# Performance work log

Measured on AMD Instinct MI355X. Metric: run time of the kernel, lower is better.

## Reference

```python
import jax, jax.numpy as jnp
import numpy as np

N = 50000      # nodes
E = 800000     # edges
IN = 64        # in_feats
HID = 4        # hidden_size
OUT = 64       # out_feats
COORS = 3
EPS = 1e-07
NEG_SLOPE = 0.01  # F.leaky_relu default


def setup_inputs() -> dict:
    key = jax.random.key(0)
    ks = jax.random.split(key, 10)
    feat = jax.random.normal(ks[0], (N, IN), dtype=jnp.float32)
    pos = jax.random.normal(ks[1], (N, COORS), dtype=jnp.float32)
    src = jax.random.randint(ks[2], (E,), 0, N, dtype=jnp.int32)
    dst = jax.random.randint(ks[3], (E,), 0, N, dtype=jnp.int32)
    W_self = jax.random.normal(ks[4], (OUT, IN), dtype=jnp.float32) * 0.1
    W_sp = jax.random.normal(ks[5], (HID * IN, COORS), dtype=jnp.float32) * 0.3
    b_sp = jax.random.normal(ks[6], (HID * IN,), dtype=jnp.float32) * 0.05
    W_neigh = jax.random.normal(ks[7], (OUT, HID * IN), dtype=jnp.float32) * 0.05
    b_neigh = jax.random.normal(ks[8], (OUT,), dtype=jnp.float32) * 0.05
    bias = jnp.zeros((OUT,), dtype=jnp.float32)
    return {"feat": feat, "pos": pos, "src": src, "dst": dst,
            "W_self": W_self, "W_sp": W_sp, "b_sp": b_sp,
            "W_neigh": W_neigh, "b_neigh": b_neigh, "bias": bias}


def reference(feat, pos, src, dst, W_self, W_sp, b_sp, W_neigh, b_neigh, bias):
    # per-edge spatial weighting
    rel = pos[dst] - pos[src]                                   # [E, 3]
    scal = jnp.linalg.norm(rel, axis=1, keepdims=True) + EPS    # [E, 1]
    ws = (rel + 1.0) / scal                                     # [E, 3]
    s = jax.nn.leaky_relu(ws @ W_sp.T + b_sp, NEG_SLOPE)        # [E, HID*IN]
    # modulate gathered src features: reshape(E, IN, HID) * h_src[:, :, None]
    msg = (s.reshape(E, IN, HID) * feat[src][:, :, None]).reshape(E, IN * HID)
    # mean aggregation per destination node (zero for isolated nodes)
    neigh_sum = jax.ops.segment_sum(msg, dst, num_segments=N)   # [N, IN*HID]
    cnt = jax.ops.segment_sum(jnp.ones((E,), feat.dtype), dst, num_segments=N)
    neigh_h = neigh_sum / jnp.maximum(cnt, 1.0)[:, None]
    # output projections
    h_neigh = neigh_h @ W_neigh.T + b_neigh                     # [N, OUT]
    rst = feat @ W_self.T + h_neigh + bias                      # [N, OUT]
    return rst
```

## Files before the change

### kernel.cpp

```cpp
#include <hip/hip_runtime.h>
#include <math.h>

#define N_NODES 50000
#define N_EDGES 800000
#define EPS 1e-7f
#define NEG_SLOPE 0.01f

#define BUCKET 64
#define EDGE_BLOCKS (N_EDGES / 256)
#define FEAT_BLOCKS (N_NODES * 64 / 4 / 256)

typedef __attribute__((ext_vector_type(8))) short short8;
typedef __attribute__((ext_vector_type(4))) float f32x4;

__device__ __forceinline__ unsigned bf16_rne(float x) {
    unsigned u = __float_as_uint(x);
    u += 0x7fffu + ((u >> 16) & 1u);
    return u >> 16;
}
__device__ __forceinline__ unsigned pack_bf16(float a, float b) {
    return bf16_rne(a) | (bf16_rne(b) << 16);
}


__global__ __launch_bounds__(256) void prep_kernel(
    const int* __restrict__ src, const int* __restrict__ dst,
    const float* __restrict__ pos, const float* __restrict__ feat,
    int* __restrict__ cnt, uint2* __restrict__ gdata,
    uint2* __restrict__ featb2,
    const float* __restrict__ W_neigh, const float* __restrict__ W_self,
    const float* __restrict__ b_neigh, const float* __restrict__ bias,
    unsigned* __restrict__ wnp, unsigned* __restrict__ wsp, float* __restrict__ bb)
{
    const int bid = blockIdx.x;

    if (bid < EDGE_BLOCKS) {
        const int i = bid * 256 + threadIdx.x;
        const int s = src[i], d = dst[i];
        const float sx = pos[s * 3 + 0], sy = pos[s * 3 + 1], sz = pos[s * 3 + 2];
        const float dx = pos[d * 3 + 0], dy = pos[d * 3 + 1], dz = pos[d * 3 + 2];
        const float rx = dx - sx, ry = dy - sy, rz = dz - sz;
        const float inv =
            __builtin_amdgcn_rcpf(__builtin_amdgcn_sqrtf(rx * rx + ry * ry + rz * rz) + EPS);
        const uint2 rec = make_uint2(pack_bf16((rx + 1.f) * inv, (ry + 1.f) * inv),
                                     bf16_rne((rz + 1.f) * inv) | ((unsigned)s << 16));
        const int p = atomicAdd(&cnt[d], 1);
        if (p < BUCKET) gdata[(size_t)d * BUCKET + p] = rec;
        return;
    }

    if (bid == EDGE_BLOCKS) {
        const int t = threadIdx.x;
        const float2* Wn2 = (const float2*)W_neigh;
        const float2* Ws2 = (const float2*)W_self;
        for (int i = t; i < 64 * 128; i += 256) {
            float2 v = Wn2[i];
            wnp[i] = pack_bf16(v.x, v.y);
        }
        for (int i = t; i < 64 * 32; i += 256) {
            float2 v = Ws2[i];
            wsp[i] = pack_bf16(v.x, v.y);
        }
        if (t < 64) bb[t] = b_neigh[t] + bias[t];
        return;
    }

    const int idx = (bid - EDGE_BLOCKS - 1) * 256 + threadIdx.x;
    float4 v = reinterpret_cast<const float4*>(feat)[idx];
    featb2[idx] = make_uint2(pack_bf16(v.x, v.y), pack_bf16(v.z, v.w));
}


#define ACC_STRIDE 264

__global__ __launch_bounds__(256) void aggregate_project_kernel(
    const unsigned short* __restrict__ featb, const float* __restrict__ W_sp,
    const float* __restrict__ b_sp, const int* __restrict__ cnt,
    const uint2* __restrict__ gdata, const short* __restrict__ wnb,
    const short* __restrict__ wsb, const float* __restrict__ bb,
    float* __restrict__ out)
{
    __shared__ unsigned short accS[16 * ACC_STRIDE];

    const int lane = threadIdx.x & 63;
    const int w = threadIdx.x >> 6;
    const int nb = blockIdx.x << 4;

    float wsp0[4], wsp1[4], wsp2[4], bsp[4];
#pragma unroll
    for (int h = 0; h < 4; ++h) {
        int j = lane * 4 + h;
        wsp0[h] = W_sp[j * 3 + 0];
        wsp1[h] = W_sp[j * 3 + 1];
        wsp2[h] = W_sp[j * 3 + 2];
        bsp[h]  = b_sp[j];
    }

    for (int q = 0; q < 4; ++q) {
        const int r = (w << 2) + q;
        const int n = nb + r;
        const int degt = __builtin_amdgcn_readfirstlane(cnt[n]);
        const int deg = min(degt, BUCKET);
        const uint2* gp = gdata + (size_t)n * BUCKET;

        float a0 = 0.f, a1 = 0.f, a2 = 0.f, a3 = 0.f;

        if (deg > 0) {
            const int dm = deg - 1;
            uint2 u0 = gp[0];
            uint2 u1 = gp[min(1, dm)];
            uint2 u2 = gp[min(2, dm)];
            uint2 u3 = gp[min(3, dm)];
            float f0 = __uint_as_float((unsigned)featb[(size_t)(u0.y >> 16) * 64 + lane] << 16);
            float f1 = __uint_as_float((unsigned)featb[(size_t)(u1.y >> 16) * 64 + lane] << 16);

            for (int e = 0; e < deg; e += 2) {
                uint2 u4 = gp[min(e + 4, dm)];
                uint2 u5 = gp[min(e + 5, dm)];
                float f2 = __uint_as_float((unsigned)featb[(size_t)(u2.y >> 16) * 64 + lane] << 16);
                float f3 = __uint_as_float((unsigned)featb[(size_t)(u3.y >> 16) * 64 + lane] << 16);

                {
                    const float wx = __uint_as_float(u0.x << 16);
                    const float wy = __uint_as_float(u0.x & 0xffff0000u);
                    const float wz = __uint_as_float(u0.y << 16);
                    float t0 = fmaf(wx, wsp0[0], fmaf(wy, wsp1[0], fmaf(wz, wsp2[0], bsp[0])));
                    float t1 = fmaf(wx, wsp0[1], fmaf(wy, wsp1[1], fmaf(wz, wsp2[1], bsp[1])));
                    float t2 = fmaf(wx, wsp0[2], fmaf(wy, wsp1[2], fmaf(wz, wsp2[2], bsp[2])));
                    float t3 = fmaf(wx, wsp0[3], fmaf(wy, wsp1[3], fmaf(wz, wsp2[3], bsp[3])));
                    a0 = fmaf(fmaxf(t0, t0 * NEG_SLOPE), f0, a0);
                    a1 = fmaf(fmaxf(t1, t1 * NEG_SLOPE), f0, a1);
                    a2 = fmaf(fmaxf(t2, t2 * NEG_SLOPE), f0, a2);
                    a3 = fmaf(fmaxf(t3, t3 * NEG_SLOPE), f0, a3);
                }
                {
                    const float m1 = (e + 1 <= dm) ? 1.f : 0.f;
                    const float fm = f1 * m1;
                    const float wx = __uint_as_float(u1.x << 16);
                    const float wy = __uint_as_float(u1.x & 0xffff0000u);
                    const float wz = __uint_as_float(u1.y << 16);
                    float t0 = fmaf(wx, wsp0[0], fmaf(wy, wsp1[0], fmaf(wz, wsp2[0], bsp[0])));
                    float t1 = fmaf(wx, wsp0[1], fmaf(wy, wsp1[1], fmaf(wz, wsp2[1], bsp[1])));
                    float t2 = fmaf(wx, wsp0[2], fmaf(wy, wsp1[2], fmaf(wz, wsp2[2], bsp[2])));
                    float t3 = fmaf(wx, wsp0[3], fmaf(wy, wsp1[3], fmaf(wz, wsp2[3], bsp[3])));
                    a0 = fmaf(fmaxf(t0, t0 * NEG_SLOPE), fm, a0);
                    a1 = fmaf(fmaxf(t1, t1 * NEG_SLOPE), fm, a1);
                    a2 = fmaf(fmaxf(t2, t2 * NEG_SLOPE), fm, a2);
                    a3 = fmaf(fmaxf(t3, t3 * NEG_SLOPE), fm, a3);
                }

                u0 = u2; u1 = u3; u2 = u4; u3 = u5;
                f0 = f2; f1 = f3;
            }
        }

        const float mscale = 1.f / fmaxf((float)degt, 1.f);
        uint2 pv = make_uint2(pack_bf16(a0 * mscale, a1 * mscale),
                              pack_bf16(a2 * mscale, a3 * mscale));
        *reinterpret_cast<uint2*>(&accS[r * ACC_STRIDE + lane * 4]) = pv;
    }
    __syncthreads();

    const int mrow = lane & 15;
    const int quad = lane >> 4;
    const int o = (w << 4) + mrow;

    f32x4 acc = {0.f, 0.f, 0.f, 0.f};

    const unsigned short* Ar = &accS[mrow * ACC_STRIDE + quad * 8];
    const short* Br = wnb + o * 256 + quad * 8;
#pragma unroll
    for (int ks = 0; ks < 8; ++ks) {
        short8 a = *reinterpret_cast<const short8*>(Ar + ks * 32);
        short8 b = *reinterpret_cast<const short8*>(Br + ks * 32);
        acc = __builtin_amdgcn_mfma_f32_16x16x32_bf16(a, b, acc, 0, 0, 0);
    }

    const short* Fr = (const short*)featb + (size_t)(nb + mrow) * 64 + quad * 8;
    const short* Sr = wsb + o * 64 + quad * 8;
#pragma unroll
    for (int ks = 0; ks < 2; ++ks) {
        short8 a = *reinterpret_cast<const short8*>(Fr + ks * 32);
        short8 b = *reinterpret_cast<const short8*>(Sr + ks * 32);
        acc = __builtin_amdgcn_mfma_f32_16x16x32_bf16(a, b, acc, 0, 0, 0);
    }

    const float badd = bb[o];
#pragma unroll
    for (int r = 0; r < 4; ++r) {
        out[(size_t)(nb + quad * 4 + r) * 64 + o] = acc[r] + badd;
    }
}


extern "C" void kernel_launch(void* const* d_in, const int* in_sizes, int n_in,
                              void* d_out, int out_size, void* d_ws, size_t ws_size,
                              hipStream_t stream) {
    (void)in_sizes; (void)n_in; (void)out_size; (void)ws_size;
    const float* feat    = (const float*)d_in[0];
    const float* pos     = (const float*)d_in[1];
    const int*   src     = (const int*)d_in[2];
    const int*   dst     = (const int*)d_in[3];
    const float* W_self  = (const float*)d_in[4];
    const float* W_sp    = (const float*)d_in[5];
    const float* b_sp    = (const float*)d_in[6];
    const float* W_neigh = (const float*)d_in[7];
    const float* b_neigh = (const float*)d_in[8];
    const float* bias    = (const float*)d_in[9];
    float* out = (float*)d_out;

    uint2*        gdata = (uint2*)d_ws;
    uint2*        featb2 = gdata + (size_t)N_NODES * BUCKET;
    unsigned int* wnp   = (unsigned int*)(featb2 + (size_t)N_NODES * 16);
    unsigned int* wsp   = wnp + 8192;
    float*        bb    = (float*)(wsp + 2048);
    int*          cnt   = (int*)(bb + 64);

    hipMemsetAsync(cnt, 0, N_NODES * sizeof(int), stream);
    prep_kernel<<<EDGE_BLOCKS + 1 + FEAT_BLOCKS, 256, 0, stream>>>(
        src, dst, pos, feat, cnt, gdata, featb2,
        W_neigh, W_self, b_neigh, bias, wnp, wsp, bb);
    aggregate_project_kernel<<<N_NODES / 16, 256, 0, stream>>>(
        (const unsigned short*)featb2, W_sp, b_sp, cnt, gdata,
        (const short*)wnp, (const short*)wsp, bb, out);
}
```

Baseline: 194.4 us.

## Gather fp32 features directly and pad per-node atomic counters

Removes the bf16 feature conversion pass from the prep kernel. The aggregation kernel now gathers fp32 feature rows directly and converts the self-projection fragment inline. Per-node degree counters are spaced 16 ints apart to reduce atomic contention on shared cache lines. This trades away the conversion traffic and a kernel section for doubled bytes per gathered neighbor row and a larger memset.

```diff
diff --git a/kernel.cpp b/kernel.cpp
--- a/kernel.cpp
+++ b/kernel.cpp
@@ -8,7 +8,7 @@
 
 #define BUCKET 64
 #define EDGE_BLOCKS (N_EDGES / 256)
-#define FEAT_BLOCKS (N_NODES * 64 / 4 / 256)
+#define CNT_STRIDE 16
 
 typedef __attribute__((ext_vector_type(8))) short short8;
 typedef __attribute__((ext_vector_type(4))) float f32x4;
@@ -25,29 +25,13 @@
 
 __global__ __launch_bounds__(256) void prep_kernel(
     const int* __restrict__ src, const int* __restrict__ dst,
-    const float* __restrict__ pos, const float* __restrict__ feat,
+    const float* __restrict__ pos,
     int* __restrict__ cnt, uint2* __restrict__ gdata,
-    uint2* __restrict__ featb2,
     const float* __restrict__ W_neigh, const float* __restrict__ W_self,
     const float* __restrict__ b_neigh, const float* __restrict__ bias,
     unsigned* __restrict__ wnp, unsigned* __restrict__ wsp, float* __restrict__ bb)
 {
     const int bid = blockIdx.x;
-
-    if (bid < EDGE_BLOCKS) {
-        const int i = bid * 256 + threadIdx.x;
-        const int s = src[i], d = dst[i];
-        const float sx = pos[s * 3 + 0], sy = pos[s * 3 + 1], sz = pos[s * 3 + 2];
-        const float dx = pos[d * 3 + 0], dy = pos[d * 3 + 1], dz = pos[d * 3 + 2];
-        const float rx = dx - sx, ry = dy - sy, rz = dz - sz;
-        const float inv =
-            __builtin_amdgcn_rcpf(__builtin_amdgcn_sqrtf(rx * rx + ry * ry + rz * rz) + EPS);
-        const uint2 rec = make_uint2(pack_bf16((rx + 1.f) * inv, (ry + 1.f) * inv),
-                                     bf16_rne((rz + 1.f) * inv) | ((unsigned)s << 16));
-        const int p = atomicAdd(&cnt[d], 1);
-        if (p < BUCKET) gdata[(size_t)d * BUCKET + p] = rec;
-        return;
-    }
 
     if (bid == EDGE_BLOCKS) {
         const int t = threadIdx.x;
@@ -65,16 +49,35 @@
         return;
     }
 
-    const int idx = (bid - EDGE_BLOCKS - 1) * 256 + threadIdx.x;
-    float4 v = reinterpret_cast<const float4*>(feat)[idx];
-    featb2[idx] = make_uint2(pack_bf16(v.x, v.y), pack_bf16(v.z, v.w));
+    const int i = bid * 256 + threadIdx.x;
+    const int s = src[i], d = dst[i];
+    const float sx = pos[s * 3 + 0], sy = pos[s * 3 + 1], sz = pos[s * 3 + 2];
+    const float dx = pos[d * 3 + 0], dy = pos[d * 3 + 1], dz = pos[d * 3 + 2];
+    const float rx = dx - sx, ry = dy - sy, rz = dz - sz;
+    const float inv =
+        __builtin_amdgcn_rcpf(__builtin_amdgcn_sqrtf(rx * rx + ry * ry + rz * rz) + EPS);
+    const uint2 rec = make_uint2(pack_bf16((rx + 1.f) * inv, (ry + 1.f) * inv),
+                                 bf16_rne((rz + 1.f) * inv) | ((unsigned)s << 16));
+    const int p = atomicAdd(&cnt[d * CNT_STRIDE], 1);
+    if (p < BUCKET) gdata[(size_t)d * BUCKET + p] = rec;
 }
 
 
 #define ACC_STRIDE 264
 
+__device__ __forceinline__ short8 feat_frag_bf16(const float* p) {
+    float4 x0 = *reinterpret_cast<const float4*>(p);
+    float4 x1 = *reinterpret_cast<const float4*>(p + 4);
+    union { unsigned u[4]; short8 s; } c;
+    c.u[0] = pack_bf16(x0.x, x0.y);
+    c.u[1] = pack_bf16(x0.z, x0.w);
+    c.u[2] = pack_bf16(x1.x, x1.y);
+    c.u[3] = pack_bf16(x1.z, x1.w);
+    return c.s;
+}
+
 __global__ __launch_bounds__(256) void aggregate_project_kernel(
-    const unsigned short* __restrict__ featb, const float* __restrict__ W_sp,
+    const float* __restrict__ feat, const float* __restrict__ W_sp,
     const float* __restrict__ b_sp, const int* __restrict__ cnt,
     const uint2* __restrict__ gdata, const short* __restrict__ wnb,
     const short* __restrict__ wsb, const float* __restrict__ bb,
@@ -99,7 +102,7 @@
     for (int q = 0; q < 4; ++q) {
         const int r = (w << 2) + q;
         const int n = nb + r;
-        const int degt = __builtin_amdgcn_readfirstlane(cnt[n]);
+        const int degt = __builtin_amdgcn_readfirstlane(cnt[n * CNT_STRIDE]);
         const int deg = min(degt, BUCKET);
         const uint2* gp = gdata + (size_t)n * BUCKET;
 
@@ -111,14 +114,14 @@
             uint2 u1 = gp[min(1, dm)];
             uint2 u2 = gp[min(2, dm)];
             uint2 u3 = gp[min(3, dm)];
-            float f0 = __uint_as_float((unsigned)featb[(size_t)(u0.y >> 16) * 64 + lane] << 16);
-            float f1 = __uint_as_float((unsigned)featb[(size_t)(u1.y >> 16) * 64 + lane] << 16);
+            float f0 = feat[(size_t)(u0.y >> 16) * 64 + lane];
+            float f1 = feat[(size_t)(u1.y >> 16) * 64 + lane];
 
             for (int e = 0; e < deg; e += 2) {
                 uint2 u4 = gp[min(e + 4, dm)];
                 uint2 u5 = gp[min(e + 5, dm)];
-                float f2 = __uint_as_float((unsigned)featb[(size_t)(u2.y >> 16) * 64 + lane] << 16);
-                float f3 = __uint_as_float((unsigned)featb[(size_t)(u3.y >> 16) * 64 + lane] << 16);
+                float f2 = feat[(size_t)(u2.y >> 16) * 64 + lane];
+                float f3 = feat[(size_t)(u3.y >> 16) * 64 + lane];
 
                 {
                     const float wx = __uint_as_float(u0.x << 16);
@@ -176,11 +179,11 @@
         acc = __builtin_amdgcn_mfma_f32_16x16x32_bf16(a, b, acc, 0, 0, 0);
     }
 
-    const short* Fr = (const short*)featb + (size_t)(nb + mrow) * 64 + quad * 8;
+    const float* Fr = feat + (size_t)(nb + mrow) * 64 + quad * 8;
     const short* Sr = wsb + o * 64 + quad * 8;
 #pragma unroll
     for (int ks = 0; ks < 2; ++ks) {
-        short8 a = *reinterpret_cast<const short8*>(Fr + ks * 32);
+        short8 a = feat_frag_bf16(Fr + ks * 32);
         short8 b = *reinterpret_cast<const short8*>(Sr + ks * 32);
         acc = __builtin_amdgcn_mfma_f32_16x16x32_bf16(a, b, acc, 0, 0, 0);
     }
@@ -210,17 +213,14 @@
     float* out = (float*)d_out;
 
     uint2*        gdata = (uint2*)d_ws;
-    uint2*        featb2 = gdata + (size_t)N_NODES * BUCKET;
-    unsigned int* wnp   = (unsigned int*)(featb2 + (size_t)N_NODES * 16);
+    unsigned int* wnp   = (unsigned int*)(gdata + (size_t)N_NODES * BUCKET);
     unsigned int* wsp   = wnp + 8192;
     float*        bb    = (float*)(wsp + 2048);
     int*          cnt   = (int*)(bb + 64);
 
-    hipMemsetAsync(cnt, 0, N_NODES * sizeof(int), stream);
-    prep_kernel<<<EDGE_BLOCKS + 1 + FEAT_BLOCKS, 256, 0, stream>>>(
-        src, dst, pos, feat, cnt, gdata, featb2,
-        W_neigh, W_self, b_neigh, bias, wnp, wsp, bb);
+    hipMemsetAsync(cnt, 0, (size_t)N_NODES * CNT_STRIDE * sizeof(int), stream);
+    prep_kernel<<<EDGE_BLOCKS + 1, 256, 0, stream>>>(
+        src, dst, pos, cnt, gdata, W_neigh, W_self, b_neigh, bias, wnp, wsp, bb);
     aggregate_project_kernel<<<N_NODES / 16, 256, 0, stream>>>(
-        (const unsigned short*)featb2, W_sp, b_sp, cnt, gdata,
-        (const short*)wnp, (const short*)wsp, bb, out);
-}
+        feat, W_sp, b_sp, cnt, gdata, (const short*)wnp, (const short*)wsp, bb, out);
+}
```

After: 200.6 us. 1.03x slower.
